# Performance work log

Measured on AMD Instinct MI355X. Metric: run time of the kernel, lower is better.

Reference implementation:

```python
import jax, jax.numpy as jnp
import numpy as np

B, S, D_MODEL, N_HEADS, D_K, D_V = 4, 1024, 1024, 16, 64, 64


def setup_inputs() -> dict:
    key = jax.random.key(0)
    ks = jax.random.split(key, 6)
    # xavier-normal std for [d_model, n_heads*d_k] weight
    std = float(np.sqrt(2.0 / (D_MODEL + N_HEADS * D_K)))
    return {
        "q": jax.random.normal(ks[0], (B, S, D_MODEL), jnp.float32),
        "k": jax.random.normal(ks[1], (B, S, D_MODEL), jnp.float32),
        "v": jax.random.normal(ks[2], (B, S, D_MODEL), jnp.float32),
        "w_q": jax.random.normal(ks[3], (D_MODEL, N_HEADS * D_K), jnp.float32) * std,
        "w_k": jax.random.normal(ks[4], (D_MODEL, N_HEADS * D_K), jnp.float32) * std,
        "w_v": jax.random.normal(ks[5], (D_MODEL, N_HEADS * D_V), jnp.float32) * std,
        "b_q": jnp.zeros((N_HEADS * D_K,), jnp.float32),
        "b_k": jnp.zeros((N_HEADS * D_K,), jnp.float32),
        "b_v": jnp.zeros((N_HEADS * D_V,), jnp.float32),
        "attn_mask": 0,  # falsy -> no masking, matching `if attn_mask:` in source
    }


def reference(q, k, v, w_q, w_k, w_v, b_q, b_k, b_v, attn_mask):
    b = q.shape[0]
    scale = jnp.sqrt(jnp.float32(D_K))
    # QKV projections -> [b, heads, seq, d]
    q_s = (q @ w_q + b_q).reshape(b, -1, N_HEADS, D_K).transpose(0, 2, 1, 3)
    k_s = (k @ w_k + b_k).reshape(b, -1, N_HEADS, D_K).transpose(0, 2, 1, 3)
    v_s = (v @ w_v + b_v).reshape(b, -1, N_HEADS, D_V).transpose(0, 2, 1, 3)
    scores = jnp.einsum("bhqd,bhkd->bhqk", q_s, k_s) / scale
    attn = jax.nn.softmax(scores, axis=-1)
    context = jnp.einsum("bhqk,bhkd->bhqd", attn, v_s)
    context = context.transpose(0, 2, 1, 3).reshape(b, -1, N_HEADS * D_V)
    return context, attn
```

## Files before the change

### kernel.cpp

```cpp
#include <hip/hip_runtime.h>

typedef unsigned short u16;
typedef __bf16 bf16x8 __attribute__((ext_vector_type(8)));
typedef float f32x4 __attribute__((ext_vector_type(4)));

__device__ __forceinline__ u16 f2b(float f) {
  unsigned u = __float_as_uint(f);
  return (u16)((u + 0x7FFFu + ((u >> 16) & 1u)) >> 16);
}
__device__ __forceinline__ float bl(unsigned w) { return __uint_as_float(w << 16); }
__device__ __forceinline__ float bh(unsigned w) { return __uint_as_float(w & 0xFFFF0000u); }

__device__ __forceinline__ void lds_load16(const void* g, void* l) {
  __builtin_amdgcn_global_load_lds(
      (__attribute__((address_space(1))) void*)(void*)g,
      (__attribute__((address_space(3))) void*)l, 16, 0, 0);
}

__global__ __launch_bounds__(256) void cvt_qkv(
    const float4* __restrict__ q, const float4* __restrict__ k, const float4* __restrict__ v,
    u16* __restrict__ qb, u16* __restrict__ kb, u16* __restrict__ vb) {
  int idx = blockIdx.x * 256 + threadIdx.x;
  int which = idx >> 20;
  int i = idx & 0xFFFFF;
  const float4* src = which == 0 ? q : which == 1 ? k : v;
  u16* dst = which == 0 ? qb : which == 1 ? kb : vb;
  float4 f = src[i];
  ushort4 o;
  o.x = f2b(f.x); o.y = f2b(f.y); o.z = f2b(f.z); o.w = f2b(f.w);
  *(ushort4*)(dst + (size_t)i * 4) = o;
}

__global__ __launch_bounds__(256) void transpose_cvt(
    const float* __restrict__ wq, const float* __restrict__ wk, const float* __restrict__ wv,
    u16* __restrict__ oq, u16* __restrict__ ok, u16* __restrict__ ov) {
  __shared__ float tile[32][33];
  int z = blockIdx.z;
  const float* in = z == 0 ? wq : z == 1 ? wk : wv;
  u16* out = z == 0 ? oq : z == 1 ? ok : ov;
  int x = blockIdx.x * 32 + threadIdx.x;
  for (int i = 0; i < 32; i += 8) {
    int y = blockIdx.y * 32 + threadIdx.y + i;
    tile[threadIdx.y + i][threadIdx.x] = in[(size_t)y * 1024 + x];
  }
  __syncthreads();
  int x2 = blockIdx.y * 32 + threadIdx.x;
  for (int i = 0; i < 32; i += 8) {
    int y2 = blockIdx.x * 32 + threadIdx.y + i;
    out[(size_t)y2 * 1024 + x2] = f2b(tile[threadIdx.x][threadIdx.y + i]);
  }
}

__global__ __launch_bounds__(256) void proj_gemm(
    const u16* __restrict__ qb, const u16* __restrict__ kb, const u16* __restrict__ vb,
    const u16* __restrict__ wqT, const u16* __restrict__ wkT, const u16* __restrict__ wvT,
    const float* __restrict__ bq, const float* __restrict__ bk, const float* __restrict__ bv,
    u16* __restrict__ q_s, u16* __restrict__ k_s, u16* __restrict__ vT_s) {
  __shared__ __align__(16) u16 As[128 * 64];
  __shared__ __align__(16) u16 Bs[128 * 64];
  const int z = blockIdx.z;
  const u16* A = z == 0 ? qb : z == 1 ? kb : vb;
  const u16* W = z == 0 ? wqT : z == 1 ? wkT : wvT;
  const float* bias = z == 0 ? bq : z == 1 ? bk : bv;

  const int t = threadIdx.x, lane = t & 63, wave = t >> 6;
  const int m0 = blockIdx.y * 128, n0 = blockIdx.x * 128;
  const int wm = (wave >> 1) * 64, wn = (wave & 1) * 64;

  f32x4 acc[4][4] = {};

  for (int k0 = 0; k0 < 1024; k0 += 64) {
    __syncthreads();
    #pragma unroll
    for (int r = 0; r < 4; ++r) {
      int flat = t + r * 256;
      int row = flat >> 3, gidx = (flat & 7) ^ (row & 7);
      lds_load16(A + (size_t)(m0 + row) * 1024 + k0 + gidx * 8, As + (size_t)flat * 8);
    }
    #pragma unroll
    for (int r = 0; r < 4; ++r) {
      int flat = t + r * 256;
      int row = flat >> 3, gidx = (flat & 7) ^ (row & 7);
      lds_load16(W + (size_t)(n0 + row) * 1024 + k0 + gidx * 8, Bs + (size_t)flat * 8);
    }
    __syncthreads();
    #pragma unroll
    for (int ks = 0; ks < 2; ++ks) {
      int kg = ks * 4 + (lane >> 4);
      bf16x8 af[4], bf[4];
      #pragma unroll
      for (int mi = 0; mi < 4; ++mi) {
        int rm = wm + mi * 16 + (lane & 15);
        af[mi] = *(const bf16x8*)(As + rm * 64 + ((kg ^ (rm & 7)) * 8));
      }
      #pragma unroll
      for (int ni = 0; ni < 4; ++ni) {
        int rn = wn + ni * 16 + (lane & 15);
        bf[ni] = *(const bf16x8*)(Bs + rn * 64 + ((kg ^ (rn & 7)) * 8));
      }
      #pragma unroll
      for (int mi = 0; mi < 4; ++mi)
        #pragma unroll
        for (int ni = 0; ni < 4; ++ni)
          acc[mi][ni] = __builtin_amdgcn_mfma_f32_16x16x32_bf16(af[mi], bf[ni], acc[mi][ni], 0, 0, 0);
    }
  }

  const float scale = (z == 0) ? 0.125f : 1.0f;
  #pragma unroll
  for (int mi = 0; mi < 4; ++mi) {
    #pragma unroll
    for (int ni = 0; ni < 4; ++ni) {
      int colb = n0 + wn + ni * 16 + (lane & 15);
      float bsv = bias[colb];
      int rowb0 = m0 + wm + mi * 16 + (lane >> 4) * 4;
      if (z == 2) {
        int bb = rowb0 >> 10, s0 = rowb0 & 1023;
        int hh = colb >> 6, dd = colb & 63;
        ushort4 o;
        o.x = f2b(acc[mi][ni][0] + bsv); o.y = f2b(acc[mi][ni][1] + bsv);
        o.z = f2b(acc[mi][ni][2] + bsv); o.w = f2b(acc[mi][ni][3] + bsv);
        *(ushort4*)(vT_s + ((((size_t)bb * 16 + hh) * 64 + dd) << 10) + s0) = o;
      } else {
        u16* dst = (z == 0) ? q_s : k_s;
        #pragma unroll
        for (int r = 0; r < 4; ++r)
          dst[(size_t)(rowb0 + r) * 1024 + colb] = f2b((acc[mi][ni][r] + bsv) * scale);
      }
    }
  }
}

__global__ __launch_bounds__(512, 2) void attn_kernel(
    const u16* __restrict__ q_s, const u16* __restrict__ k_s,
    const u16* __restrict__ vT_s, float* __restrict__ out_ctx,
    float* __restrict__ out_attn) {
  __shared__ __align__(16) u16 kv[2 * 64 * 64];
  __shared__ __align__(16) u16 sc[64 * 1024];
  __shared__ float red[128];
  __shared__ float inv[64];

  const int t = threadIdx.x, lane = t & 63, wave = t >> 6;
  const int bhd = blockIdx.x;
  const int b = bhd >> 4, h = bhd & 15;
  const int m0 = blockIdx.y * 64;
  const int mt = wave & 3;
  const int nh2 = wave >> 2;
  const int l15 = lane & 15, lg = lane >> 4;

  bf16x8 af[2];
  {
    int row = mt * 16 + l15;
    const u16* qp = q_s + (size_t)(b * 1024 + m0 + row) * 1024 + h * 64;
    af[0] = *(const bf16x8*)(qp + lg * 8);
    af[1] = *(const bf16x8*)(qp + 32 + lg * 8);
  }

  {
    int row = t >> 3, g = t & 7, gx = g ^ (row & 7);
    lds_load16(k_s + ((size_t)(b * 1024 + row) * 1024 + h * 64 + gx * 8),
               kv + (size_t)t * 8);
  }
  float sums[4] = {0.f, 0.f, 0.f, 0.f};
  for (int c = 0; c < 16; ++c) {
    __syncthreads();
    if (c < 15) {
      int row = t >> 3, g = t & 7, gx = g ^ (row & 7);
      lds_load16(k_s + ((size_t)(b * 1024 + (c + 1) * 64 + row) * 1024 + h * 64 + gx * 8),
                 kv + ((c + 1) & 1) * 4096 + (size_t)t * 8);
    }
    const u16* kb = kv + (c & 1) * 4096;
    f32x4 a4[2] = {};
    #pragma unroll
    for (int ks = 0; ks < 2; ++ks) {
      #pragma unroll
      for (int ni = 0; ni < 2; ++ni) {
        int n = nh2 * 32 + ni * 16 + l15;
        bf16x8 bf = *(const bf16x8*)(kb + n * 64 + (((ks * 4 + lg) ^ (n & 7)) * 8));
        a4[ni] = __builtin_amdgcn_mfma_f32_16x16x32_bf16(af[ks], bf, a4[ni], 0, 0, 0);
      }
    }
    #pragma unroll
    for (int ni = 0; ni < 2; ++ni) {
      int colc = nh2 * 32 + ni * 16 + l15;
      int gi = colc >> 3, e7 = colc & 7;
      #pragma unroll
      for (int r = 0; r < 4; ++r) {
        int row = mt * 16 + lg * 4 + r;
        float e = __expf(a4[ni][r]);
        sums[r] += e;
        sc[row * 1024 + c * 64 + ((gi ^ (row & 7)) * 8) + e7] = f2b(e);
      }
    }
  }

  #pragma unroll
  for (int m = 1; m <= 8; m <<= 1)
    #pragma unroll
    for (int r = 0; r < 4; ++r) sums[r] += __shfl_xor(sums[r], m, 64);
  if (l15 == 0) {
    #pragma unroll
    for (int r = 0; r < 4; ++r) red[wave * 16 + lg * 4 + r] = sums[r];
  }
  __syncthreads();
  if (t < 64) inv[t] = 1.0f / (red[t] + red[64 + t]);
  __syncthreads();

  {
    int row = t >> 3, g = t & 7, gx = g ^ (row & 7);
    lds_load16(vT_s + ((size_t)(bhd * 64 + row) * 1024 + gx * 8), kv + (size_t)t * 8);
  }
  f32x4 acc2[2] = {};
  const size_t attn_row0 = (size_t)bhd * 1024 + m0;
  for (int c = 0; c < 16; ++c) {
    __syncthreads();
    if (c < 15) {
      int row = t >> 3, g = t & 7, gx = g ^ (row & 7);
      lds_load16(vT_s + ((size_t)(bhd * 64 + row) * 1024 + (c + 1) * 64 + gx * 8),
                 kv + ((c + 1) & 1) * 4096 + (size_t)t * 8);
    }
    {
      int row = t >> 3, g = t & 7;
      const u16* p = sc + row * 1024 + c * 64 + ((g ^ (row & 7)) * 8);
      uint4 pk = *(const uint4*)p;
      float is = inv[row];
      f32x4 o0, o1;
      o0[0] = bl(pk.x) * is; o0[1] = bh(pk.x) * is; o0[2] = bl(pk.y) * is; o0[3] = bh(pk.y) * is;
      o1[0] = bl(pk.z) * is; o1[1] = bh(pk.z) * is; o1[2] = bl(pk.w) * is; o1[3] = bh(pk.w) * is;
      float* dst = out_attn + ((attn_row0 + row) << 10) + c * 64 + g * 8;
      __builtin_nontemporal_store(o0, (f32x4*)dst);
      __builtin_nontemporal_store(o1, (f32x4*)(dst + 4));
    }
    const u16* vb = kv + (c & 1) * 4096;
    #pragma unroll
    for (int ks = 0; ks < 2; ++ks) {
      int mr = mt * 16 + l15;
      bf16x8 pa = *(const bf16x8*)(sc + mr * 1024 + c * 64 + (((ks * 4 + lg) ^ (mr & 7)) * 8));
      #pragma unroll
      for (int ni = 0; ni < 2; ++ni) {
        int d = nh2 * 32 + ni * 16 + l15;
        bf16x8 bf = *(const bf16x8*)(vb + d * 64 + (((ks * 4 + lg) ^ (d & 7)) * 8));
        acc2[ni] = __builtin_amdgcn_mfma_f32_16x16x32_bf16(pa, bf, acc2[ni], 0, 0, 0);
      }
    }
  }
  #pragma unroll
  for (int ni = 0; ni < 2; ++ni) {
    int d = nh2 * 32 + ni * 16 + l15;
    #pragma unroll
    for (int r = 0; r < 4; ++r) {
      int row = mt * 16 + lg * 4 + r;
      out_ctx[(size_t)(b * 1024 + m0 + row) * 1024 + h * 64 + d] = acc2[ni][r] * inv[row];
    }
  }
}

extern "C" void kernel_launch(void* const* d_in, const int* in_sizes, int n_in,
                              void* d_out, int out_size, void* d_ws, size_t ws_size,
                              hipStream_t stream) {
  const float* q  = (const float*)d_in[0];
  const float* k  = (const float*)d_in[1];
  const float* v  = (const float*)d_in[2];
  const float* wq = (const float*)d_in[3];
  const float* wk = (const float*)d_in[4];
  const float* wv = (const float*)d_in[5];
  const float* bq = (const float*)d_in[6];
  const float* bk = (const float*)d_in[7];
  const float* bv = (const float*)d_in[8];

  float* out_ctx  = (float*)d_out;
  float* out_attn = out_ctx + (size_t)4 * 1024 * 1024;

  u16* qb  = (u16*)d_ws;
  u16* kb  = qb  + (size_t)4194304;
  u16* vb  = kb  + (size_t)4194304;
  u16* wqT = vb  + (size_t)4194304;
  u16* wkT = wqT + (size_t)1048576;
  u16* wvT = wkT + (size_t)1048576;
  u16* q_s = wvT + (size_t)1048576;
  u16* k_s = q_s + (size_t)4194304;
  u16* vT  = k_s + (size_t)4194304;

  cvt_qkv<<<dim3(12288), 256, 0, stream>>>((const float4*)q, (const float4*)k,
                                           (const float4*)v, qb, kb, vb);
  transpose_cvt<<<dim3(32, 32, 3), dim3(32, 8), 0, stream>>>(wq, wk, wv, wqT, wkT, wvT);
  proj_gemm<<<dim3(8, 32, 3), 256, 0, stream>>>(qb, kb, vb, wqT, wkT, wvT,
                                                bq, bk, bv, q_s, k_s, vT);
  attn_kernel<<<dim3(64, 16), 512, 0, stream>>>(q_s, k_s, vT, out_ctx, out_attn);
}
```

Measured before the change: 459.3 us.

## Halve attention tile to 32 rows to fit two blocks per CU

Shrinks the attention block from 64 query rows and 512 threads to 32 rows and 256 threads. This halves the shared-memory score buffer, so two blocks can share a CU instead of one. K/V double buffering is replaced by a single buffer with extra barriers, and s_setprio is raised around the MFMA sections. The cost is that each K/V tile is loaded by twice as many blocks, and the prefetch of the next tile no longer overlaps with compute.

```diff
diff --git a/kernel.cpp b/kernel.cpp
--- a/kernel.cpp
+++ b/kernel.cpp
@@ -131,21 +131,21 @@
   }
 }
 
-__global__ __launch_bounds__(512, 2) void attn_kernel(
+__global__ __launch_bounds__(256, 2) void attn_kernel(
     const u16* __restrict__ q_s, const u16* __restrict__ k_s,
     const u16* __restrict__ vT_s, float* __restrict__ out_ctx,
     float* __restrict__ out_attn) {
-  __shared__ __align__(16) u16 kv[2 * 64 * 64];
-  __shared__ __align__(16) u16 sc[64 * 1024];
-  __shared__ float red[128];
-  __shared__ float inv[64];
+  __shared__ __align__(16) u16 kv[64 * 64];
+  __shared__ __align__(16) u16 sc[32 * 1024];
+  __shared__ float red[4 * 32];
+  __shared__ float inv[32];
 
   const int t = threadIdx.x, lane = t & 63, wave = t >> 6;
   const int bhd = blockIdx.x;
   const int b = bhd >> 4, h = bhd & 15;
-  const int m0 = blockIdx.y * 64;
-  const int mt = wave & 3;
-  const int nh2 = wave >> 2;
+  const int m0 = blockIdx.y * 32;
+  const int mt = wave & 1;
+  const int nh2 = wave >> 1;
   const int l15 = lane & 15, lg = lane >> 4;
 
   bf16x8 af[2];
@@ -156,30 +156,28 @@
     af[1] = *(const bf16x8*)(qp + 32 + lg * 8);
   }
 
-  {
-    int row = t >> 3, g = t & 7, gx = g ^ (row & 7);
-    lds_load16(k_s + ((size_t)(b * 1024 + row) * 1024 + h * 64 + gx * 8),
-               kv + (size_t)t * 8);
-  }
   float sums[4] = {0.f, 0.f, 0.f, 0.f};
   for (int c = 0; c < 16; ++c) {
-    __syncthreads();
-    if (c < 15) {
-      int row = t >> 3, g = t & 7, gx = g ^ (row & 7);
-      lds_load16(k_s + ((size_t)(b * 1024 + (c + 1) * 64 + row) * 1024 + h * 64 + gx * 8),
-                 kv + ((c + 1) & 1) * 4096 + (size_t)t * 8);
-    }
-    const u16* kb = kv + (c & 1) * 4096;
+    #pragma unroll
+    for (int r = 0; r < 2; ++r) {
+      int flat = t + r * 256;
+      int row = flat >> 3, g = flat & 7, gx = g ^ (row & 7);
+      lds_load16(k_s + ((size_t)(b * 1024 + c * 64 + row) * 1024 + h * 64 + gx * 8),
+                 kv + (size_t)flat * 8);
+    }
+    __syncthreads();
     f32x4 a4[2] = {};
+    __builtin_amdgcn_s_setprio(1);
     #pragma unroll
     for (int ks = 0; ks < 2; ++ks) {
       #pragma unroll
       for (int ni = 0; ni < 2; ++ni) {
         int n = nh2 * 32 + ni * 16 + l15;
-        bf16x8 bf = *(const bf16x8*)(kb + n * 64 + (((ks * 4 + lg) ^ (n & 7)) * 8));
+        bf16x8 bf = *(const bf16x8*)(kv + n * 64 + (((ks * 4 + lg) ^ (n & 7)) * 8));
         a4[ni] = __builtin_amdgcn_mfma_f32_16x16x32_bf16(af[ks], bf, a4[ni], 0, 0, 0);
       }
     }
+    __builtin_amdgcn_s_setprio(0);
     #pragma unroll
     for (int ni = 0; ni < 2; ++ni) {
       int colc = nh2 * 32 + ni * 16 + l15;
@@ -192,6 +190,7 @@
         sc[row * 1024 + c * 64 + ((gi ^ (row & 7)) * 8) + e7] = f2b(e);
       }
     }
+    __syncthreads();
   }
 
   #pragma unroll
@@ -200,24 +199,24 @@
     for (int r = 0; r < 4; ++r) sums[r] += __shfl_xor(sums[r], m, 64);
   if (l15 == 0) {
     #pragma unroll
-    for (int r = 0; r < 4; ++r) red[wave * 16 + lg * 4 + r] = sums[r];
+    for (int r = 0; r < 4; ++r) red[wave * 32 + mt * 16 + lg * 4 + r] = sums[r];
   }
   __syncthreads();
-  if (t < 64) inv[t] = 1.0f / (red[t] + red[64 + t]);
+  if (t < 32) {
+    int w0 = t >> 4;
+    inv[t] = 1.0f / (red[w0 * 32 + t] + red[(w0 + 2) * 32 + t]);
+  }
   __syncthreads();
 
-  {
-    int row = t >> 3, g = t & 7, gx = g ^ (row & 7);
-    lds_load16(vT_s + ((size_t)(bhd * 64 + row) * 1024 + gx * 8), kv + (size_t)t * 8);
-  }
   f32x4 acc2[2] = {};
   const size_t attn_row0 = (size_t)bhd * 1024 + m0;
   for (int c = 0; c < 16; ++c) {
-    __syncthreads();
-    if (c < 15) {
-      int row = t >> 3, g = t & 7, gx = g ^ (row & 7);
-      lds_load16(vT_s + ((size_t)(bhd * 64 + row) * 1024 + (c + 1) * 64 + gx * 8),
-                 kv + ((c + 1) & 1) * 4096 + (size_t)t * 8);
+    #pragma unroll
+    for (int r = 0; r < 2; ++r) {
+      int flat = t + r * 256;
+      int row = flat >> 3, g = flat & 7, gx = g ^ (row & 7);
+      lds_load16(vT_s + ((size_t)(bhd * 64 + row) * 1024 + c * 64 + gx * 8),
+                 kv + (size_t)flat * 8);
     }
     {
       int row = t >> 3, g = t & 7;
@@ -231,7 +230,8 @@
       __builtin_nontemporal_store(o0, (f32x4*)dst);
       __builtin_nontemporal_store(o1, (f32x4*)(dst + 4));
     }
-    const u16* vb = kv + (c & 1) * 4096;
+    __syncthreads();
+    __builtin_amdgcn_s_setprio(1);
     #pragma unroll
     for (int ks = 0; ks < 2; ++ks) {
       int mr = mt * 16 + l15;
@@ -239,10 +239,12 @@
       #pragma unroll
       for (int ni = 0; ni < 2; ++ni) {
         int d = nh2 * 32 + ni * 16 + l15;
-        bf16x8 bf = *(const bf16x8*)(vb + d * 64 + (((ks * 4 + lg) ^ (d & 7)) * 8));
+        bf16x8 bf = *(const bf16x8*)(kv + d * 64 + (((ks * 4 + lg) ^ (d & 7)) * 8));
         acc2[ni] = __builtin_amdgcn_mfma_f32_16x16x32_bf16(pa, bf, acc2[ni], 0, 0, 0);
       }
     }
+    __builtin_amdgcn_s_setprio(0);
+    __syncthreads();
   }
   #pragma unroll
   for (int ni = 0; ni < 2; ++ni) {
@@ -286,5 +288,5 @@
   transpose_cvt<<<dim3(32, 32, 3), dim3(32, 8), 0, stream>>>(wq, wk, wv, wqT, wkT, wvT);
   proj_gemm<<<dim3(8, 32, 3), 256, 0, stream>>>(qb, kb, vb, wqT, wkT, wvT,
                                                 bq, bk, bv, q_s, k_s, vT);
-  attn_kernel<<<dim3(64, 16), 512, 0, stream>>>(q_s, k_s, vT, out_ctx, out_attn);
-}
+  attn_kernel<<<dim3(64, 32), 256, 0, stream>>>(q_s, k_s, vT, out_ctx, out_attn);
+}
```

New measurement: 462.0 us. About the same (+0.6%).
